# Kernel tuning notes

Hardware: AMD Instinct MI355X
Metric: run time of the kernel (lower is better)

The kernel has to match this reference:

```python
import jax, jax.numpy as jnp
import numpy as np

N, D, F, H, DH, R = 50000, 16, 256, 8, 32, 20
HOP_NUM, TOP_K, ALPHA, NEG_SLOPE = 10, 5, 0.1, 0.2
FF_HID = 4 * F


def _ln(x, g, b, eps=1e-5):
    m = x.mean(-1, keepdims=True)
    v = ((x - m) ** 2).mean(-1, keepdims=True)
    return (x - m) / jnp.sqrt(v + eps) * g + b


def setup_inputs() -> dict:
    key = jax.random.key(0)
    ks = jax.random.split(key, 16)
    s = 0.02
    inp = {
        'ent_feat': jax.random.normal(ks[0], (N, F), jnp.float32),
        'rel_feat': jax.random.normal(ks[1], (R, F), jnp.float32),
        'W_head': jax.random.normal(ks[2], (F, H * DH), jnp.float32) * s,
        'W_tail': jax.random.normal(ks[3], (F, H * DH), jnp.float32) * s,
        'W_ent': jax.random.normal(ks[4], (F, H * DH), jnp.float32) * s,
        'W_rel': jax.random.normal(ks[5], (F, H * DH), jnp.float32) * s,
        'attn_h': jax.random.normal(ks[6], (H, DH), jnp.float32) * s,
        'attn_t': jax.random.normal(ks[7], (H, DH), jnp.float32) * s,
        'attn_r': jax.random.normal(ks[8], (H, DH), jnp.float32) * s,
        'ln_ent_g': jnp.ones((F,), jnp.float32), 'ln_ent_b': jnp.zeros((F,), jnp.float32),
        'ln_rel_g': jnp.ones((F,), jnp.float32), 'ln_rel_b': jnp.zeros((F,), jnp.float32),
        'ln_ff_g': jnp.ones((F,), jnp.float32), 'ln_ff_b': jnp.zeros((F,), jnp.float32),
        'ffn_W1': jax.random.normal(ks[9], (F, FF_HID), jnp.float32) * s,
        'ffn_b1': jnp.zeros((FF_HID,), jnp.float32),
        'ffn_W2': jax.random.normal(ks[10], (FF_HID, F), jnp.float32) * s,
        'ffn_b2': jnp.zeros((F,), jnp.float32),
        'src': jax.random.randint(ks[11], (N, D), 0, N, jnp.int32),
        'rid': jax.random.randint(ks[12], (N, D), 0, R, jnp.int32),
    }
    return inp


def reference(ent_feat, rel_feat, W_head, W_tail, W_ent, W_rel,
              attn_h, attn_t, attn_r,
              ln_ent_g, ln_ent_b, ln_rel_g, ln_rel_b, ln_ff_g, ln_ff_b,
              ffn_W1, ffn_b1, ffn_W2, ffn_b2, src, rid):
    # --- projections (dropout = 0 at eval) ---
    x = _ln(ent_feat, ln_ent_g, ln_ent_b)                    # [N,F]
    fh = (x @ W_head).reshape(N, H, DH)
    ftl = (x @ W_tail).reshape(N, H, DH)
    fe = (x @ W_ent).reshape(N, H, DH)                       # 'ft' messages
    r = _ln(rel_feat, ln_rel_g, ln_rel_b)
    fr = (r @ W_rel).reshape(R, H, DH)
    # --- per-node / per-relation attention logits ---
    eh = (fh * attn_h).sum(-1)                               # [N,H]
    et = (ftl * attn_t).sum(-1)                              # [N,H]
    er = (fr * attn_r).sum(-1)                               # [R,H]
    # edges: row i = incoming edges of dst node i, sources src[i,:]
    e = eh[src] + et[:, None, :] + er[rid]                   # [N,D,H]
    e = jnp.where(e > 0, e, NEG_SLOPE * e)                   # LeakyReLU
    # --- edge_softmax over incoming edges of each dst node ---
    a = jax.nn.softmax(e, axis=1)                            # [N,D,H]
    # --- top-k sparsification + renormalization ---
    a_t = a.transpose(0, 2, 1)                               # [N,H,D]
    topv, _ = jax.lax.top_k(a_t, TOP_K)                      # [N,H,K]
    kth = topv[..., TOP_K - 1]                               # [N,H]
    top_sum = topv.sum(-1)                                   # [N,H]
    a_n = jnp.where(a_t >= kth[..., None], a_t, 0.0) / top_sum[..., None]  # [N,H,D]
    # --- PPR diffusion: feat <- (1-a) * A @ feat + a * feat0 ---
    feat0 = fe

    def step(feat, _):
        m = feat[src]                                        # [N,D,H,DH]
        agg = jnp.einsum('ndhk,nhd->nhk', m, a_n)            # [N,H,DH]
        return (1.0 - ALPHA) * agg + ALPHA * feat0, None

    feat, _ = jax.lax.scan(step, feat0, None, length=HOP_NUM)
    # --- residual (Identity since in==out) + FFN block ---
    rst = feat + ent_feat.reshape(N, H, DH)
    rst = rst.reshape(N, F)
    y = _ln(rst, ln_ff_g, ln_ff_b)
    ff = jax.nn.relu(y @ ffn_W1 + ffn_b1) @ ffn_W2 + ffn_b2
    return ff + rst
```

## Files before the change

### kernel.cpp

```cpp
#include <hip/hip_runtime.h>

#define NN   50000
#define DD   16
#define FFE  256
#define HH   8
#define DHH  32
#define RR   20
#define HOPN 10

typedef unsigned short u16;
typedef unsigned int   u32;
typedef __attribute__((ext_vector_type(8))) short  short8;
typedef __attribute__((ext_vector_type(4))) float  floatx4;

__device__ __forceinline__ float b2f(u16 u){ return __uint_as_float(((u32)u)<<16); }
__device__ __forceinline__ u16 f2b(float f){
  u32 x = __float_as_uint(f);
  u32 r = (x + 0x7fffu + ((x>>16)&1u)) >> 16;
  return (u16)r;
}
__device__ __forceinline__ float blo(u32 u){ return __uint_as_float(u << 16); }
__device__ __forceinline__ float bhi(u32 u){ return __uint_as_float(u & 0xffff0000u); }

__global__ __launch_bounds__(256) void castw_kernel(
    const float* __restrict__ We, const float* __restrict__ W1,
    const float* __restrict__ W2,
    u16* __restrict__ Wet, u16* __restrict__ W1t, u16* __restrict__ W2t)
{
  int tid = blockIdx.x*256 + threadIdx.x;
  if (tid < 256*256) {
    int k = tid >> 8, n = tid & 255;
    Wet[n*256 + k] = f2b(We[tid]);
  } else if (tid < 256*256 + 256*1024) {
    int s = tid - 65536;
    int k = s >> 10, n = s & 1023;
    W1t[n*256 + k] = f2b(W1[s]);
  } else if (tid < 589824) {
    int s = tid - 327680;
    int k = s >> 8, n = s & 255;
    W2t[n*1024 + k] = f2b(W2[s]);
  }
}

__global__ __launch_bounds__(256) void prep_kernel(
    const float* __restrict__ rel_feat,
    const float* __restrict__ W_head, const float* __restrict__ W_tail,
    const float* __restrict__ W_rel,
    const float* __restrict__ attn_h, const float* __restrict__ attn_t,
    const float* __restrict__ attn_r,
    const float* __restrict__ lng, const float* __restrict__ lnb,
    double* __restrict__ Wc, double* __restrict__ er)
{
  int t = threadIdx.x;
  if (blockIdx.x == RR) {
    for (int h = 0; h < HH; h++) {
      double sh = 0.0, st = 0.0;
      #pragma unroll
      for (int c = 0; c < DHH; c++) {
        int j = h*DHH + c;
        sh += (double)W_head[t*FFE + j] * (double)attn_h[j];
        st += (double)W_tail[t*FFE + j] * (double)attn_t[j];
      }
      Wc[t*16 + h]     = sh;
      Wc[t*16 + 8 + h] = st;
    }
    return;
  }
  int r = blockIdx.x;
  __shared__ double red[8];
  __shared__ double rln[256];
  double v = (double)rel_feat[r*FFE + t];
  double s = v, q = v*v;
  #pragma unroll
  for (int o = 32; o; o >>= 1) { s += __shfl_xor(s, o, 64); q += __shfl_xor(q, o, 64); }
  if ((t & 63) == 0) { red[t>>6] = s; red[4 + (t>>6)] = q; }
  __syncthreads();
  double stot = red[0]+red[1]+red[2]+red[3];
  double qtot = red[4]+red[5]+red[6]+red[7];
  double mean = stot * (1.0/256.0);
  double var  = qtot * (1.0/256.0) - mean*mean;
  double rstd = 1.0 / sqrt(var + 1e-5);
  rln[t] = (v - mean) * rstd * (double)lng[t] + (double)lnb[t];
  __syncthreads();
  double acc = 0.0;
  for (int k = 0; k < 256; k++) acc += rln[k] * (double)W_rel[k*FFE + t];
  double p = acc * (double)attn_r[t];
  #pragma unroll
  for (int o = 16; o; o >>= 1) p += __shfl_down(p, o, 32);
  if ((t & 31) == 0) er[r*HH + (t>>5)] = p;
}

__global__ __launch_bounds__(256) void logits_kernel(
    const float* __restrict__ ent,
    const float* __restrict__ lng, const float* __restrict__ lnb,
    const double* __restrict__ Wc,
    u16* __restrict__ xb, double* __restrict__ eh, double* __restrict__ et)
{
  int tid = threadIdx.x;
  int w = tid >> 6, l = tid & 63;
  int rowA = blockIdx.x*8 + w*2;
  int rowB = rowA + 1;
  float gg[4], bbv[4];
  #pragma unroll
  for (int j = 0; j < 4; j++) { gg[j] = lng[l + 64*j]; bbv[j] = lnb[l + 64*j]; }
  double xA[4], xB[4];
  #pragma unroll
  for (int j = 0; j < 4; j++) xA[j] = (double)ent[(size_t)rowA*FFE + l + 64*j];
  #pragma unroll
  for (int j = 0; j < 4; j++) xB[j] = (double)ent[(size_t)rowB*FFE + l + 64*j];
  double sA = xA[0]+xA[1]+xA[2]+xA[3];
  double sB = xB[0]+xB[1]+xB[2]+xB[3];
  double qA = xA[0]*xA[0]+xA[1]*xA[1]+xA[2]*xA[2]+xA[3]*xA[3];
  double qB = xB[0]*xB[0]+xB[1]*xB[1]+xB[2]*xB[2]+xB[3]*xB[3];
  #pragma unroll
  for (int o = 32; o; o >>= 1) {
    sA += __shfl_xor(sA, o, 64); qA += __shfl_xor(qA, o, 64);
    sB += __shfl_xor(sB, o, 64); qB += __shfl_xor(qB, o, 64);
  }
  double mA = sA * (1.0/256.0), mB = sB * (1.0/256.0);
  double vA = qA * (1.0/256.0) - mA*mA, vB = qB * (1.0/256.0) - mB*mB;
  double rsA = 1.0 / sqrt(vA + 1e-5), rsB = 1.0 / sqrt(vB + 1e-5);
  #pragma unroll
  for (int j = 0; j < 4; j++) {
    double yA = (xA[j]-mA)*rsA*(double)gg[j] + (double)bbv[j];
    double yB = (xB[j]-mB)*rsB*(double)gg[j] + (double)bbv[j];
    xA[j] = yA; xB[j] = yB;
    xb[(size_t)rowA*FFE + l + 64*j] = f2b((float)yA);
    xb[(size_t)rowB*FFE + l + 64*j] = f2b((float)yB);
  }
  double accA[16], accB[16];
  #pragma unroll
  for (int o = 0; o < 16; o++) { accA[o] = 0.0; accB[o] = 0.0; }
  #pragma unroll
  for (int j = 0; j < 4; j++) {
    int k = l + 64*j;
    const double2* wp = (const double2*)(Wc + (size_t)k*16);
    double wv[16];
    #pragma unroll
    for (int u = 0; u < 8; u++) { double2 tv = wp[u]; wv[2*u] = tv.x; wv[2*u+1] = tv.y; }
    #pragma unroll
    for (int o = 0; o < 16; o++) {
      accA[o] = fma(xA[j], wv[o], accA[o]);
      accB[o] = fma(xB[j], wv[o], accB[o]);
    }
  }
  int b0 = l & 1, b1 = (l>>1)&1, b2 = (l>>2)&1, b3 = (l>>3)&1;
  double r1A[8], r1B[8];
  #pragma unroll
  for (int s = 0; s < 8; s++) {
    double kA = b0 ? accA[8+s] : accA[s];
    double dA = b0 ? accA[s]   : accA[8+s];
    double kB = b0 ? accB[8+s] : accB[s];
    double dB = b0 ? accB[s]   : accB[8+s];
    r1A[s] = kA + __shfl_xor(dA, 1, 64);
    r1B[s] = kB + __shfl_xor(dB, 1, 64);
  }
  double r2A[4], r2B[4];
  #pragma unroll
  for (int s = 0; s < 4; s++) {
    double kA = b1 ? r1A[4+s] : r1A[s];
    double dA = b1 ? r1A[s]   : r1A[4+s];
    double kB = b1 ? r1B[4+s] : r1B[s];
    double dB = b1 ? r1B[s]   : r1B[4+s];
    r2A[s] = kA + __shfl_xor(dA, 2, 64);
    r2B[s] = kB + __shfl_xor(dB, 2, 64);
  }
  double r3A[2], r3B[2];
  #pragma unroll
  for (int s = 0; s < 2; s++) {
    double kA = b2 ? r2A[2+s] : r2A[s];
    double dA = b2 ? r2A[s]   : r2A[2+s];
    double kB = b2 ? r2B[2+s] : r2B[s];
    double dB = b2 ? r2B[s]   : r2B[2+s];
    r3A[s] = kA + __shfl_xor(dA, 4, 64);
    r3B[s] = kB + __shfl_xor(dB, 4, 64);
  }
  double k4A = b3 ? r3A[1] : r3A[0];
  double d4A = b3 ? r3A[0] : r3A[1];
  double k4B = b3 ? r3B[1] : r3B[0];
  double d4B = b3 ? r3B[0] : r3B[1];
  double fA4 = k4A + __shfl_xor(d4A, 8, 64);
  double fB4 = k4B + __shfl_xor(d4B, 8, 64);
  fA4 += __shfl_xor(fA4, 16, 64);  fB4 += __shfl_xor(fB4, 16, 64);
  fA4 += __shfl_xor(fA4, 32, 64);  fB4 += __shfl_xor(fB4, 32, 64);
  int o = (b0<<3) | (b1<<2) | (b2<<1) | b3;
  if (l < 16) {
    if (o < 8) eh[(size_t)rowA*HH + o] = fA4;
    else       et[(size_t)rowA*HH + (o-8)] = fA4;
  } else if (l < 32) {
    if (o < 8) eh[(size_t)rowB*HH + o] = fB4;
    else       et[(size_t)rowB*HH + (o-8)] = fB4;
  }
}

template<int EPI>
__global__ __launch_bounds__(256) void gemm_kernel(
    const u16* __restrict__ A, const u16* __restrict__ B,
    const float* __restrict__ bias,
    const u16* __restrict__ feat, const float* __restrict__ ent,
    u16* __restrict__ Obf, float* __restrict__ Of,
    int M, int N, int K)
{
  __shared__ u16 As[128][40];
  __shared__ u16 Bs[128][40];
  int t = threadIdx.x;
  int i0 = blockIdx.x * 128;
  int n0 = blockIdx.y * 128;
  int w = t >> 6, l = t & 63;
  int cr = t >> 2;
  int cc = (t & 3) * 8;
  int ga0 = min(i0 + cr, M-1);
  int ga1 = min(i0 + cr + 64, M-1);
  int gb0 = n0 + cr;
  int gb1 = n0 + cr + 64;
  floatx4 acc[2][8];
  #pragma unroll
  for (int mt = 0; mt < 2; mt++)
    #pragma unroll
    for (int nt = 0; nt < 8; nt++) acc[mt][nt] = (floatx4){0.f,0.f,0.f,0.f};
  int ln = l & 15, lq = (l >> 4) * 8;
  for (int k0 = 0; k0 < K; k0 += 32) {
    __syncthreads();
    *(uint4*)&As[cr][cc]      = *(const uint4*)&A[(size_t)ga0*K + k0 + cc];
    *(uint4*)&As[cr+64][cc]   = *(const uint4*)&A[(size_t)ga1*K + k0 + cc];
    *(uint4*)&Bs[cr][cc]      = *(const uint4*)&B[(size_t)gb0*K + k0 + cc];
    *(uint4*)&Bs[cr+64][cc]   = *(const uint4*)&B[(size_t)gb1*K + k0 + cc];
    __syncthreads();
    short8 bfr[8];
    #pragma unroll
    for (int nt = 0; nt < 8; nt++) bfr[nt] = *(const short8*)&Bs[nt*16 + ln][lq];
    #pragma unroll
    for (int mt = 0; mt < 2; mt++) {
      short8 afr = *(const short8*)&As[w*32 + mt*16 + ln][lq];
      #pragma unroll
      for (int nt = 0; nt < 8; nt++)
        acc[mt][nt] = __builtin_amdgcn_mfma_f32_16x16x32_bf16(afr, bfr[nt], acc[mt][nt], 0, 0, 0);
    }
  }
  int lr = (l >> 4) * 4;
  #pragma unroll
  for (int mt = 0; mt < 2; mt++) {
    #pragma unroll
    for (int nt = 0; nt < 8; nt++) {
      int col = n0 + nt*16 + ln;
      #pragma unroll
      for (int r = 0; r < 4; r++) {
        int row = i0 + w*32 + mt*16 + lr + r;
        if (row < M) {
          float v = acc[mt][nt][r];
          if (EPI == 0) {
            Obf[(size_t)row*N + col] = f2b(v);
          } else if (EPI == 1) {
            v += bias[col];
            Obf[(size_t)row*N + col] = f2b(v > 0.f ? v : 0.f);
          } else {
            v += bias[col] + b2f(feat[(size_t)row*FFE + col]) + ent[(size_t)row*FFE + col];
            Of[(size_t)row*N + col] = v;
          }
        }
      }
    }
  }
}

__global__ __launch_bounds__(256) void edge_kernel(
    const int* __restrict__ src, const int* __restrict__ rid,
    const double* __restrict__ eh, const double* __restrict__ et,
    const double* __restrict__ er,
    uint4* __restrict__ rec)
{
  int tid = blockIdx.x*256 + threadIdx.x;
  if (tid >= NN*HH) return;
  int i = tid >> 3, h = tid & 7;
  double bet = et[tid];
  double e[16]; int sj[16];
  #pragma unroll
  for (int d = 0; d < 16; d++) {
    int s = src[i*DD + d];
    int rv = rid[i*DD + d];
    sj[d] = s;
    double v = eh[s*HH + h] + bet + er[rv*HH + h];
    e[d] = (v > 0.0) ? v : 0.2 * v;
  }
  u32 mask = 0; double vs[5]; int js[5];
  #pragma unroll
  for (int k = 0; k < 5; k++) {
    double best = -1e300; int bj = 0, bd = 0;
    #pragma unroll
    for (int d = 0; d < 16; d++) {
      bool c = (((mask>>d)&1u) == 0u) && (e[d] > best);
      if (c) { best = e[d]; bj = sj[d]; bd = d; }
    }
    mask |= (1u << bd); vs[k] = best; js[k] = bj;
  }
  double kth = vs[4];
  int j6 = 0; bool f6 = false;
  #pragma unroll
  for (int d = 0; d < 16; d++) {
    if ((((mask>>d)&1u) == 0u) && (e[d] == kth) && !f6) { j6 = sj[d]; f6 = true; }
  }
  float m0 = (float)vs[0];
  float ex[5], ssum = 0.f;
  #pragma unroll
  for (int k = 0; k < 5; k++) { ex[k] = __expf((float)vs[k] - m0); ssum += ex[k]; }
  float inv = 0.9f / ssum;
  float w5 = f6 ? ex[4]*inv : 0.f;
  size_t rb = (size_t)tid * 4;
  rec[rb+0] = make_uint4((u32)js[0], (u32)js[1], (u32)js[2], (u32)js[3]);
  rec[rb+1] = make_uint4((u32)js[4], (u32)j6,
                         __float_as_uint(ex[0]*inv), __float_as_uint(ex[1]*inv));
  rec[rb+2] = make_uint4(__float_as_uint(ex[2]*inv), __float_as_uint(ex[3]*inv),
                         __float_as_uint(ex[4]*inv), __float_as_uint(w5));
}

__global__ __launch_bounds__(256) void diff_kernel(
    const u16* __restrict__ fold, const u16* __restrict__ fe,
    const uint4* __restrict__ rec, u16* __restrict__ fnew)
{
  int tid = threadIdx.x;
  int g = tid >> 2, q = tid & 3;
  int i = blockIdx.x*8 + (g >> 3);
  int h = g & 7;
  const uint4* f4  = (const uint4*)fold;
  const uint4* fe4 = (const uint4*)fe;
  uint4* fn4 = (uint4*)fnew;
  size_t rb = ((size_t)i*HH + h) * 4;
  uint4 ra = rec[rb], rbv = rec[rb+1], rc = rec[rb+2];
  int idx[6] = {(int)ra.x,(int)ra.y,(int)ra.z,(int)ra.w,(int)rbv.x,(int)rbv.y};
  float wv[6];
  wv[0]=__uint_as_float(rbv.z); wv[1]=__uint_as_float(rbv.w);
  wv[2]=__uint_as_float(rc.x);  wv[3]=__uint_as_float(rc.y);
  wv[4]=__uint_as_float(rc.z);  wv[5]=__uint_as_float(rc.w);
  int co = h*4 + q;
  uint4 fv = fe4[(size_t)i*32 + co];
  float a0 = 0.1f*blo(fv.x), a1 = 0.1f*bhi(fv.x);
  float a2 = 0.1f*blo(fv.y), a3 = 0.1f*bhi(fv.y);
  float a4 = 0.1f*blo(fv.z), a5 = 0.1f*bhi(fv.z);
  float a6 = 0.1f*blo(fv.w), a7 = 0.1f*bhi(fv.w);
  #pragma unroll
  for (int k = 0; k < 5; k++) {
    uint4 v = f4[(size_t)idx[k]*32 + co];
    float wk = wv[k];
    a0 += wk*blo(v.x); a1 += wk*bhi(v.x);
    a2 += wk*blo(v.y); a3 += wk*bhi(v.y);
    a4 += wk*blo(v.z); a5 += wk*bhi(v.z);
    a6 += wk*blo(v.w); a7 += wk*bhi(v.w);
  }
  if (wv[5] != 0.f) {
    uint4 v = f4[(size_t)idx[5]*32 + co];
    float wk = wv[5];
    a0 += wk*blo(v.x); a1 += wk*bhi(v.x);
    a2 += wk*blo(v.y); a3 += wk*bhi(v.y);
    a4 += wk*blo(v.z); a5 += wk*bhi(v.z);
    a6 += wk*blo(v.w); a7 += wk*bhi(v.w);
  }
  uint4 o;
  o.x = (u32)f2b(a0) | ((u32)f2b(a1) << 16);
  o.y = (u32)f2b(a2) | ((u32)f2b(a3) << 16);
  o.z = (u32)f2b(a4) | ((u32)f2b(a5) << 16);
  o.w = (u32)f2b(a6) | ((u32)f2b(a7) << 16);
  fn4[(size_t)i*32 + co] = o;
}

__global__ __launch_bounds__(256) void ln_ff_kernel(
    const u16* __restrict__ feat, const float* __restrict__ ent,
    const float* __restrict__ g, const float* __restrict__ b,
    u16* __restrict__ y)
{
  int w = threadIdx.x >> 6, l = threadIdx.x & 63;
  int row = blockIdx.x*4 + w;
  float4 e4 = *(const float4*)&ent[row*FFE + l*4];
  ushort4 fv = *(const ushort4*)&feat[row*FFE + l*4];
  float v0 = b2f(fv.x)+e4.x, v1 = b2f(fv.y)+e4.y;
  float v2 = b2f(fv.z)+e4.z, v3 = b2f(fv.w)+e4.w;
  float s = v0+v1+v2+v3;
  float q = v0*v0 + v1*v1 + v2*v2 + v3*v3;
  #pragma unroll
  for (int o = 32; o; o >>= 1) { s += __shfl_xor(s, o, 64); q += __shfl_xor(q, o, 64); }
  float mean = s * (1.f/256.f);
  float var  = q * (1.f/256.f) - mean*mean;
  float rstd = rsqrtf(var + 1e-5f);
  float4 g4 = *(const float4*)&g[l*4];
  float4 b4 = *(const float4*)&b[l*4];
  ushort4 o4;
  o4.x = f2b((v0-mean)*rstd*g4.x + b4.x);
  o4.y = f2b((v1-mean)*rstd*g4.y + b4.y);
  o4.z = f2b((v2-mean)*rstd*g4.z + b4.z);
  o4.w = f2b((v3-mean)*rstd*g4.w + b4.w);
  *(ushort4*)&y[row*FFE + l*4] = o4;
}

extern "C" void kernel_launch(void* const* d_in, const int* in_sizes, int n_in,
                              void* d_out, int out_size, void* d_ws, size_t ws_size,
                              hipStream_t stream)
{
  const float* ent      = (const float*)d_in[0];
  const float* rel      = (const float*)d_in[1];
  const float* W_head   = (const float*)d_in[2];
  const float* W_tail   = (const float*)d_in[3];
  const float* W_ent    = (const float*)d_in[4];
  const float* W_rel    = (const float*)d_in[5];
  const float* attn_h   = (const float*)d_in[6];
  const float* attn_t   = (const float*)d_in[7];
  const float* attn_r   = (const float*)d_in[8];
  const float* ln_ent_g = (const float*)d_in[9];
  const float* ln_ent_b = (const float*)d_in[10];
  const float* ln_rel_g = (const float*)d_in[11];
  const float* ln_rel_b = (const float*)d_in[12];
  const float* ln_ff_g  = (const float*)d_in[13];
  const float* ln_ff_b  = (const float*)d_in[14];
  const float* W1       = (const float*)d_in[15];
  const float* b1       = (const float*)d_in[16];
  const float* W2       = (const float*)d_in[17];
  const float* b2       = (const float*)d_in[18];
  const int* src        = (const int*)d_in[19];
  const int* rid        = (const int*)d_in[20];
  float* out = (float*)d_out;

  char* w = (char*)d_ws;
  double* er64 = (double*)(w + 0);
  double* Wc   = (double*)(w + 4096);
  double* eh64 = (double*)(w + 36864);
  double* et64 = (double*)(w + 3236864);
  u16*    xb   = (u16*)  (w + 6436864);
  uint4*  rec  = (uint4*)(w + 6436864);
  u16*    fe   = (u16*)  (w + 32036864);
  u16*    fA   = (u16*)  (w + 57636864);
  u16*    h1   = (u16*)  (w + 0);
  u16*    fB   = (u16*)  (w + 102436864);
  u16*    y    = (u16*)  (w + 128036864);
  u16*    Wet  = (u16*)  (w + 153636864);
  u16*    W1t  = (u16*)  (w + 153767936);
  u16*    W2t  = (u16*)  (w + 154292224);

  castw_kernel<<<2304, 256, 0, stream>>>(W_ent, W1, W2, Wet, W1t, W2t);
  prep_kernel<<<RR+1, 256, 0, stream>>>(rel, W_head, W_tail, W_rel,
                                        attn_h, attn_t, attn_r,
                                        ln_rel_g, ln_rel_b, Wc, er64);
  logits_kernel<<<NN/8, 256, 0, stream>>>(ent, ln_ent_g, ln_ent_b, Wc,
                                          xb, eh64, et64);
  {
    dim3 g((NN + 127)/128, 2);
    gemm_kernel<0><<<g, 256, 0, stream>>>(xb, Wet, nullptr, nullptr, nullptr,
                                          fe, nullptr, NN, 256, 256);
  }
  edge_kernel<<<(NN*HH + 255)/256, 256, 0, stream>>>(src, rid, eh64, et64, er64,
                                                     rec);
  const u16* cur = fe;
  u16* bufs[2] = { fA, fB };
  for (int hop = 0; hop < HOPN; hop++) {
    u16* nxt = bufs[hop & 1];
    diff_kernel<<<NN/8, 256, 0, stream>>>(cur, fe, rec, nxt);
    cur = nxt;
  }
  ln_ff_kernel<<<NN/4, 256, 0, stream>>>(cur, ent, ln_ff_g, ln_ff_b, y);
  {
    dim3 g((NN + 127)/128, 8);
    gemm_kernel<1><<<g, 256, 0, stream>>>(y, W1t, b1, nullptr, nullptr,
                                          h1, nullptr, NN, 1024, 256);
  }
  {
    dim3 g((NN + 127)/128, 2);
    gemm_kernel<2><<<g, 256, 0, stream>>>(h1, W2t, b2, cur, ent,
                                          nullptr, out, NN, 256, 1024);
  }
}
```

Measured before the change: 896.8 us.

## Store diffusion features head-major so per-head gathers stay cache-resident

Features are stored as separate per-head [N,32] slabs, and the diffusion kernel is regridded so each block processes one head for 64 nodes. This keeps each hop's random gathers within a 3.2 MB slab, aiming to improve L2/last-level cache hit rates over the node-major layout. Record and self-feature reads use nontemporal loads to avoid polluting cache. The projection GEMM epilogue, LN and final GEMM epilogue are adapted to the new layout, at the cost of less contiguous writes and reads there.

```diff
diff --git a/kernel.cpp b/kernel.cpp
--- a/kernel.cpp
+++ b/kernel.cpp
@@ -7,11 +7,13 @@
 #define DHH  32
 #define RR   20
 #define HOPN 10
+#define HRS  1600000
 
 typedef unsigned short u16;
 typedef unsigned int   u32;
 typedef __attribute__((ext_vector_type(8))) short  short8;
 typedef __attribute__((ext_vector_type(4))) float  floatx4;
+typedef __attribute__((ext_vector_type(4))) unsigned int uintx4;
 
 __device__ __forceinline__ float b2f(u16 u){ return __uint_as_float(((u32)u)<<16); }
 __device__ __forceinline__ u16 f2b(float f){
@@ -253,9 +255,13 @@
           } else if (EPI == 1) {
             v += bias[col];
             Obf[(size_t)row*N + col] = f2b(v > 0.f ? v : 0.f);
+          } else if (EPI == 2) {
+            v += bias[col]
+               + b2f(feat[(size_t)(col>>5)*HRS + (size_t)row*32 + (col&31)])
+               + ent[(size_t)row*FFE + col];
+            Of[(size_t)row*N + col] = v;
           } else {
-            v += bias[col] + b2f(feat[(size_t)row*FFE + col]) + ent[(size_t)row*FFE + col];
-            Of[(size_t)row*N + col] = v;
+            Obf[(size_t)(col>>5)*HRS + (size_t)row*32 + (col&31)] = f2b(v);
           }
         }
       }
@@ -315,31 +321,34 @@
 
 __global__ __launch_bounds__(256) void diff_kernel(
     const u16* __restrict__ fold, const u16* __restrict__ fe,
-    const uint4* __restrict__ rec, u16* __restrict__ fnew)
+    const uintx4* __restrict__ rec, u16* __restrict__ fnew)
 {
   int tid = threadIdx.x;
+  int h  = blockIdx.x & 7;
+  int nb = blockIdx.x >> 3;
   int g = tid >> 2, q = tid & 3;
-  int i = blockIdx.x*8 + (g >> 3);
-  int h = g & 7;
-  const uint4* f4  = (const uint4*)fold;
-  const uint4* fe4 = (const uint4*)fe;
-  uint4* fn4 = (uint4*)fnew;
+  int i = nb*64 + g;
+  if (i >= NN) return;
+  const uintx4* f4  = (const uintx4*)(fold + (size_t)h*HRS);
+  const uintx4* fe4 = (const uintx4*)(fe   + (size_t)h*HRS);
+  uintx4*       fn4 = (uintx4*)      (fnew + (size_t)h*HRS);
   size_t rb = ((size_t)i*HH + h) * 4;
-  uint4 ra = rec[rb], rbv = rec[rb+1], rc = rec[rb+2];
+  uintx4 ra  = __builtin_nontemporal_load(&rec[rb]);
+  uintx4 rbv = __builtin_nontemporal_load(&rec[rb+1]);
+  uintx4 rc  = __builtin_nontemporal_load(&rec[rb+2]);
   int idx[6] = {(int)ra.x,(int)ra.y,(int)ra.z,(int)ra.w,(int)rbv.x,(int)rbv.y};
   float wv[6];
   wv[0]=__uint_as_float(rbv.z); wv[1]=__uint_as_float(rbv.w);
   wv[2]=__uint_as_float(rc.x);  wv[3]=__uint_as_float(rc.y);
   wv[4]=__uint_as_float(rc.z);  wv[5]=__uint_as_float(rc.w);
-  int co = h*4 + q;
-  uint4 fv = fe4[(size_t)i*32 + co];
+  uintx4 fv = __builtin_nontemporal_load(&fe4[(size_t)i*4 + q]);
   float a0 = 0.1f*blo(fv.x), a1 = 0.1f*bhi(fv.x);
   float a2 = 0.1f*blo(fv.y), a3 = 0.1f*bhi(fv.y);
   float a4 = 0.1f*blo(fv.z), a5 = 0.1f*bhi(fv.z);
   float a6 = 0.1f*blo(fv.w), a7 = 0.1f*bhi(fv.w);
   #pragma unroll
   for (int k = 0; k < 5; k++) {
-    uint4 v = f4[(size_t)idx[k]*32 + co];
+    uintx4 v = f4[(size_t)idx[k]*4 + q];
     float wk = wv[k];
     a0 += wk*blo(v.x); a1 += wk*bhi(v.x);
     a2 += wk*blo(v.y); a3 += wk*bhi(v.y);
@@ -347,30 +356,31 @@
     a6 += wk*blo(v.w); a7 += wk*bhi(v.w);
   }
   if (wv[5] != 0.f) {
-    uint4 v = f4[(size_t)idx[5]*32 + co];
+    uintx4 v = f4[(size_t)idx[5]*4 + q];
     float wk = wv[5];
     a0 += wk*blo(v.x); a1 += wk*bhi(v.x);
     a2 += wk*blo(v.y); a3 += wk*bhi(v.y);
     a4 += wk*blo(v.z); a5 += wk*bhi(v.z);
     a6 += wk*blo(v.w); a7 += wk*bhi(v.w);
   }
-  uint4 o;
+  uintx4 o;
   o.x = (u32)f2b(a0) | ((u32)f2b(a1) << 16);
   o.y = (u32)f2b(a2) | ((u32)f2b(a3) << 16);
   o.z = (u32)f2b(a4) | ((u32)f2b(a5) << 16);
   o.w = (u32)f2b(a6) | ((u32)f2b(a7) << 16);
-  fn4[(size_t)i*32 + co] = o;
+  fn4[(size_t)i*4 + q] = o;
 }
 
 __global__ __launch_bounds__(256) void ln_ff_kernel(
-    const u16* __restrict__ feat, const float* __restrict__ ent,
+    const u16* __restrict__ featH, const float* __restrict__ ent,
     const float* __restrict__ g, const float* __restrict__ b,
     u16* __restrict__ y)
 {
   int w = threadIdx.x >> 6, l = threadIdx.x & 63;
   int row = blockIdx.x*4 + w;
-  float4 e4 = *(const float4*)&ent[row*FFE + l*4];
-  ushort4 fv = *(const ushort4*)&feat[row*FFE + l*4];
+  int hh = l >> 3, c = (l & 7) * 4;
+  float4 e4 = *(const float4*)&ent[(size_t)row*FFE + l*4];
+  ushort4 fv = *(const ushort4*)&featH[(size_t)hh*HRS + (size_t)row*32 + c];
   float v0 = b2f(fv.x)+e4.x, v1 = b2f(fv.y)+e4.y;
   float v2 = b2f(fv.z)+e4.z, v3 = b2f(fv.w)+e4.w;
   float s = v0+v1+v2+v3;
@@ -387,7 +397,7 @@
   o4.y = f2b((v1-mean)*rstd*g4.y + b4.y);
   o4.z = f2b((v2-mean)*rstd*g4.z + b4.z);
   o4.w = f2b((v3-mean)*rstd*g4.w + b4.w);
-  *(ushort4*)&y[row*FFE + l*4] = o4;
+  *(ushort4*)&y[(size_t)row*FFE + l*4] = o4;
 }
 
 extern "C" void kernel_launch(void* const* d_in, const int* in_sizes, int n_in,
@@ -424,10 +434,10 @@
   double* et64 = (double*)(w + 3236864);
   u16*    xb   = (u16*)  (w + 6436864);
   uint4*  rec  = (uint4*)(w + 6436864);
-  u16*    fe   = (u16*)  (w + 32036864);
-  u16*    fA   = (u16*)  (w + 57636864);
+  u16*    feH  = (u16*)  (w + 32036864);
+  u16*    fAH  = (u16*)  (w + 57636864);
   u16*    h1   = (u16*)  (w + 0);
-  u16*    fB   = (u16*)  (w + 102436864);
+  u16*    fBH  = (u16*)  (w + 102436864);
   u16*    y    = (u16*)  (w + 128036864);
   u16*    Wet  = (u16*)  (w + 153636864);
   u16*    W1t  = (u16*)  (w + 153767936);
@@ -441,16 +451,16 @@
                                           xb, eh64, et64);
   {
     dim3 g((NN + 127)/128, 2);
-    gemm_kernel<0><<<g, 256, 0, stream>>>(xb, Wet, nullptr, nullptr, nullptr,
-                                          fe, nullptr, NN, 256, 256);
+    gemm_kernel<3><<<g, 256, 0, stream>>>(xb, Wet, nullptr, nullptr, nullptr,
+                                          feH, nullptr, NN, 256, 256);
   }
   edge_kernel<<<(NN*HH + 255)/256, 256, 0, stream>>>(src, rid, eh64, et64, er64,
                                                      rec);
-  const u16* cur = fe;
-  u16* bufs[2] = { fA, fB };
+  const u16* cur = feH;
+  u16* bufs[2] = { fAH, fBH };
   for (int hop = 0; hop < HOPN; hop++) {
     u16* nxt = bufs[hop & 1];
-    diff_kernel<<<NN/8, 256, 0, stream>>>(cur, fe, rec, nxt);
+    diff_kernel<<<782*8, 256, 0, stream>>>(cur, feH, (const uintx4*)rec, nxt);
     cur = nxt;
   }
   ln_ff_kernel<<<NN/4, 256, 0, stream>>>(cur, ent, ln_ff_g, ln_ff_b, y);
```

Measured after the change: 903.8 us. Within noise of the previous version (+0.8%).
